# Performance work log

Hardware: AMD Instinct MI355X
Metric: run time of the kernel (lower is better)

## Reference

```python
import jax, jax.numpy as jnp
import numpy as np
from math import factorial

# (mul, l, parity) per irrep; parity +1 = even (e), -1 = odd (o)
IRREPS_IN  = [(64, 0, 1), (32, 1, -1), (16, 2, 1)]
IRREPS_OUT = [(64, 0, 1), (32, 1, -1), (16, 2, 1)]
B = 20000


def _su2_cg(j1, m1, j2, m2, j3, m3):
    # Standard SU(2) Clebsch-Gordan coefficient <j1 m1 j2 m2 | j3 m3> (integer j).
    if m3 != m1 + m2:
        return 0.0
    vmin = max(-j1 + j2 + m3, -j1 + m1, 0)
    vmax = min(j2 + j3 + m1, j3 - j1 + j2, j3 + m3)
    if vmax < vmin:
        return 0.0
    f = factorial
    C = ((2 * j3 + 1) * f(j3 + j1 - j2) * f(j3 - j1 + j2) * f(j1 + j2 - j3)
         * f(j3 + m3) * f(j3 - m3)
         / (f(j1 + j2 + j3 + 1) * f(j1 - m1) * f(j1 + m1) * f(j2 - m2) * f(j2 + m2))) ** 0.5
    S = 0.0
    for v in range(vmin, vmax + 1):
        S += ((-1.0) ** (v + j2 + m2) * f(j2 + j3 + m1 - v) * f(j1 - m1 + v)
              / (f(v) * f(j3 - j1 + j2 - v) * f(j3 + m3 - v) * f(v + j1 - j2 - m3)))
    return C * S


def _q(l):
    # Real -> complex spherical-harmonics change of basis, phased so real CG is real (e3nn convention).
    q = np.zeros((2 * l + 1, 2 * l + 1), dtype=np.complex128)
    for m in range(-l, 0):
        q[l + m, l + abs(m)] = 2 ** -0.5
        q[l + m, l - abs(m)] = -1j * 2 ** -0.5
    q[l, l] = 1.0
    for m in range(1, l + 1):
        q[l + m, l + abs(m)] = (-1) ** m * 2 ** -0.5
        q[l + m, l - abs(m)] = 1j * (-1) ** m * 2 ** -0.5
    return (-1j) ** l * q


def _clebsch_gordan(l1, l2, l3):
    # Real-basis CG coefficients, shape (2l1+1, 2l2+1, 2l3+1).
    C = np.zeros((2 * l1 + 1, 2 * l2 + 1, 2 * l3 + 1), dtype=np.complex128)
    for m1 in range(-l1, l1 + 1):
        for m2 in range(-l2, l2 + 1):
            for m3 in range(-l3, l3 + 1):
                C[l1 + m1, l2 + m2, l3 + m3] = _su2_cg(l1, m1, l2, m2, l3, m3)
    Q1, Q2, Q3 = _q(l1), _q(l2), _q(l3)
    Cr = np.einsum('ij,kl,mn,ikn->jlm', Q1, Q2, np.conj(Q3.T), C)
    return np.real(Cr)


def _build():
    # Enumerate all allowed 'uvw' CG paths (i1, i2, i_out); one learned weight per path.
    ins, cgs = [], []
    for i1, (m1, l1, p1) in enumerate(IRREPS_IN):
        for i2, (m2, l2, p2) in enumerate(IRREPS_IN):
            for lo in range(abs(l1 - l2), l1 + l2 + 1):
                po = p1 * p2
                for io, (mo, l3, p3) in enumerate(IRREPS_OUT):
                    if l3 == lo and p3 == po:
                        ins.append((i1, i2, io, (m1, m2, mo)))
                        # 'component' normalization: scale so each output component has unit variance per path
                        cgs.append((_clebsch_gordan(l1, l2, l3) * (2 * l3 + 1) ** 0.5).astype(np.float32))
                        break
    fan = {}
    for (i1, i2, io, (m1, m2, mo)) in ins:
        fan[io] = fan.get(io, 0) + m1 * m2
    alphas = [1.0 / float(np.sqrt(fan[io])) for (_, _, io, _) in ins]
    return ins, cgs, alphas


INSTRUCTIONS, CGS, ALPHAS = _build()  # 11 instructions for these irreps
DIM_IN = sum(m * (2 * l + 1) for m, l, _ in IRREPS_IN)


def setup_inputs() -> dict:
    key = jax.random.key(0)
    keys = jax.random.split(key, 1 + len(INSTRUCTIONS))
    inp = {"x": jax.random.normal(keys[0], (B, DIM_IN), dtype=jnp.float32)}
    for i, (ins, k) in enumerate(zip(INSTRUCTIONS, keys[1:])):
        inp[f"w{i}"] = jax.random.normal(k, ins[3], dtype=jnp.float32)
    return inp


def _tensor_square(x, ws):
    b = x.shape[0]
    xs, off = [], 0
    for m, l, _ in IRREPS_IN:
        d = m * (2 * l + 1)
        xs.append(x[:, off:off + d].reshape(b, m, 2 * l + 1))
        off += d
    outs = [jnp.zeros((b, m, 2 * l + 1), x.dtype) for m, l, _ in IRREPS_OUT]
    for (i1, i2, io, _), w, C, a in zip(INSTRUCTIONS, ws, CGS, ALPHAS):
        # per-path weighted CG contraction: out[b,w,k] = sum_{u,v,i,j} W[u,v,w] C[i,j,k] x[b,u,i] x[b,v,j]
        contrib = jnp.einsum('uvw,ijk,bui,bvj->bwk', w, jnp.asarray(C, x.dtype),
                             xs[i1], xs[i2], optimize='optimal')
        outs[io] = outs[io] + jnp.asarray(a, x.dtype) * contrib
    return jnp.concatenate([o.reshape(b, -1) for o in outs], axis=1)


def reference(x, w0, w1, w2, w3, w4, w5, w6, w7, w8, w9, w10):
    return _tensor_square(x, (w0, w1, w2, w3, w4, w5, w6, w7, w8, w9, w10))
```

## Files before the change

kernel.cpp:

```cpp
#include <hip/hip_runtime.h>
#include <stdint.h>
#include <stddef.h>


namespace cg {

struct Cx { double re, im; };
constexpr Cx cmul(Cx a, Cx b){ return { a.re*b.re - a.im*b.im, a.re*b.im + a.im*b.re }; }

constexpr double fact(int n){ double r = 1.0; for (int i = 2; i <= n; ++i) r *= (double)i; return r; }

constexpr double csqrt(double x){
  if (x <= 0.0) return 0.0;
  double r = x > 1.0 ? x : 1.0;
  for (int i = 0; i < 50; ++i) r = 0.5*(r + x/r);
  return r;
}

constexpr double neg1pow(int k){ return (k % 2 == 0) ? 1.0 : -1.0; }

constexpr double su2_cg(int j1,int m1,int j2,int m2,int j3,int m3){
  if (m3 != m1 + m2) return 0.0;
  int vmin = -j1 + j2 + m3;
  if (-j1 + m1 > vmin) vmin = -j1 + m1;
  if (0 > vmin) vmin = 0;
  int vmax = j2 + j3 + m1;
  if (j3 - j1 + j2 < vmax) vmax = j3 - j1 + j2;
  if (j3 + m3 < vmax) vmax = j3 + m3;
  if (vmax < vmin) return 0.0;
  double C = csqrt((2.0*j3 + 1.0)*fact(j3+j1-j2)*fact(j3-j1+j2)*fact(j1+j2-j3)
                   *fact(j3+m3)*fact(j3-m3)
                   /(fact(j1+j2+j3+1)*fact(j1-m1)*fact(j1+m1)*fact(j2-m2)*fact(j2+m2)));
  double S = 0.0;
  for (int v = vmin; v <= vmax; ++v)
    S += neg1pow(v + j2 + m2)*fact(j2+j3+m1-v)*fact(j1-m1+v)
       /(fact(v)*fact(j3-j1+j2-v)*fact(j3+m3-v)*fact(v+j1-j2-m3));
  return C*S;
}

struct QM { Cx v[5][5]; };
constexpr QM qmat(int l){
  QM q{};
  const double r2 = 0.70710678118654752440;
  for (int m = -l; m < 0; ++m){
    q.v[l+m][l-m] = Cx{ r2, 0.0 };
    q.v[l+m][l+m] = Cx{ 0.0, -r2 };
  }
  q.v[l][l] = Cx{ 1.0, 0.0 };
  for (int m = 1; m <= l; ++m){
    double s = neg1pow(m)*r2;
    q.v[l+m][l+m] = Cx{ s, 0.0 };
    q.v[l+m][l-m] = Cx{ 0.0, s };
  }
  Cx ph = (l % 4 == 0) ? Cx{1,0} : (l % 4 == 1) ? Cx{0,-1} : (l % 4 == 2) ? Cx{-1,0} : Cx{0,1};
  QM out{};
  for (int i = 0; i < 5; ++i) for (int j = 0; j < 5; ++j) out.v[i][j] = cmul(ph, q.v[i][j]);
  return out;
}

struct CGT { double v[5][5][5]; };
constexpr CGT cg_tab(int l1,int l2,int l3){
  double C[5][5][5] = {};
  for (int m1 = -l1; m1 <= l1; ++m1)
    for (int m2 = -l2; m2 <= l2; ++m2)
      for (int m3 = -l3; m3 <= l3; ++m3)
        C[l1+m1][l2+m2][l3+m3] = su2_cg(l1,m1,l2,m2,l3,m3);
  QM Q1 = qmat(l1), Q2 = qmat(l2), Q3 = qmat(l3);
  const int n1 = 2*l1+1, n2 = 2*l2+1, n3 = 2*l3+1;
  const double norm = csqrt(2.0*l3 + 1.0);
  CGT R{};
  for (int j = 0; j < n1; ++j)
    for (int l = 0; l < n2; ++l)
      for (int m = 0; m < n3; ++m){
        Cx s{0,0};
        for (int i = 0; i < n1; ++i)
          for (int k = 0; k < n2; ++k)
            for (int n = 0; n < n3; ++n){
              double c = C[i][k][n];
              if (c != 0.0){
                Cx q3c{ Q3.v[n][m].re, -Q3.v[n][m].im };
                Cx t = cmul(cmul(Q1.v[i][j], Q2.v[k][l]), q3c);
                s.re += t.re*c; s.im += t.im*c;
              }
            }
        R.v[j][l][m] = s.re * norm;
      }
  return R;
}

constexpr double tab_sumsq(const CGT& t, int n1, int n2, int n3){
  double s = 0;
  for (int i = 0; i < n1; ++i) for (int j = 0; j < n2; ++j) for (int k = 0; k < n3; ++k)
    s += t.v[i][j][k]*t.v[i][j][k];
  return s;
}

}

constexpr cg::CGT T121 = cg::cg_tab(1,2,1);
constexpr cg::CGT T211 = cg::cg_tab(2,1,1);
constexpr cg::CGT T112 = cg::cg_tab(1,1,2);
constexpr cg::CGT T222 = cg::cg_tab(2,2,2);
constexpr double C000 = cg::cg_tab(0,0,0).v[0][0][0];
constexpr double C011 = cg::cg_tab(0,1,1).v[0][0][0];
constexpr double C022 = cg::cg_tab(0,2,2).v[0][0][0];
constexpr double C101 = cg::cg_tab(1,0,1).v[0][0][0];
constexpr double C110 = cg::cg_tab(1,1,0).v[0][0][0];
constexpr double C220 = cg::cg_tab(2,2,0).v[0][0][0];
constexpr double C202 = cg::cg_tab(2,0,2).v[0][0][0];

static_assert(C000 > 0.99 && C000 < 1.01, "C000");
static_assert(C011 > 1.72 && C011 < 1.74, "C011");
static_assert(C101 > 1.72 && C101 < 1.74, "C101");
static_assert(C022 > 2.22 && C022 < 2.25, "C022");
static_assert(C202 > 2.22 && C202 < 2.25, "C202");
static_assert(C110*C110 > 0.332 && C110*C110 < 0.334, "C110");
static_assert(C220*C220 > 0.199 && C220*C220 < 0.201, "C220");
static_assert(cg::tab_sumsq(T121,3,5,3) > 8.9  && cg::tab_sumsq(T121,3,5,3) < 9.1,  "T121");
static_assert(cg::tab_sumsq(T211,5,3,3) > 8.9  && cg::tab_sumsq(T211,5,3,3) < 9.1,  "T211");
static_assert(cg::tab_sumsq(T112,3,3,5) > 24.9 && cg::tab_sumsq(T112,3,3,5) < 25.1, "T112");
static_assert(cg::tab_sumsq(T222,5,5,5) > 24.9 && cg::tab_sumsq(T222,5,5,5) < 25.1, "T222");

constexpr double t121_t211_swapdiff(){
  double m = 0;
  for (int i = 0; i < 5; ++i)
    for (int j = 0; j < 3; ++j)
      for (int k = 0; k < 3; ++k){
        double d = T211.v[i][j][k] - T121.v[j][i][k];
        if (d < 0) d = -d;
        if (d > m) m = d;
      }
  return m;
}
static_assert(t121_t211_swapdiff() < 1e-9, "T211 != T121^T -- fold invalid");

constexpr double A0 = 1.0/cg::csqrt(5376.0);
constexpr double A1 = 1.0/cg::csqrt(5120.0);
constexpr double A2 = 1.0/cg::csqrt(3328.0);

constexpr double S000 = A0*C000, S110 = A0*C110, S220 = A0*C220;
constexpr double S011 = A1*C011, S101 = A1*C101, S121 = A1, S211 = A1;
constexpr double S022 = A2*C022, S112 = A2,      S202 = A2*C202, S222 = A2;

constexpr int K0 = 4352, K1 = 2560, K2 = 2304;
constexpr int WT1_OFF = 64*K0;
constexpr int WT2_OFF = WT1_OFF + 32*K1;

using short8  = __attribute__((ext_vector_type(8))) short;
using float4v = __attribute__((ext_vector_type(4))) float;

__device__ __forceinline__ unsigned pkbf(float lo, float hi){
  unsigned a = __builtin_bit_cast(unsigned, lo);
  unsigned b = __builtin_bit_cast(unsigned, hi);
  return __builtin_amdgcn_perm(b, a, 0x07060302u);
}

__device__ __forceinline__ short8 mkfrag(const float* s){
  union { short8 v; unsigned u[4]; } f;
  f.u[0] = pkbf(s[0], s[1]);
  f.u[1] = pkbf(s[2], s[3]);
  f.u[2] = pkbf(s[4], s[5]);
  f.u[3] = pkbf(s[6], s[7]);
  return f.v;
}

__device__ __forceinline__ short8 ldB(const unsigned short* p){
  return *reinterpret_cast<const short8*>(p);
}

__device__ __forceinline__ float4v MFMA(short8 a, short8 b, float4v c){
  return __builtin_amdgcn_mfma_f32_16x16x32_bf16(a, b, c, 0, 0, 0);
}

__device__ __forceinline__ unsigned short f2bf_rne(float f){
  unsigned u = __builtin_bit_cast(unsigned, f);
  u += 0x7fffu + ((u >> 16) & 1u);
  return (unsigned short)(u >> 16);
}

#define NZ(c) ((c) > 1e-12 || (c) < -1e-12)

constexpr int XS = 244;

__global__ __launch_bounds__(256)
void tsq_prep(const float* __restrict__ w0, const float* __restrict__ w1,
              const float* __restrict__ w2, const float* __restrict__ w3,
              const float* __restrict__ w4, const float* __restrict__ w5,
              const float* __restrict__ w6, const float* __restrict__ w7,
              const float* __restrict__ w8, const float* __restrict__ w9,
              const float* __restrict__ w10, unsigned short* __restrict__ wt){
  const int s   = blockIdx.x;
  const int g   = blockIdx.y;
  const int tid = threadIdx.x;

  const int lw  = 6 - g;
  const int Wn  = 1 << lw;
  const int NT  = Wn >> 4;
  int Smax;
  unsigned short* obase;
  if (g == 0){ Smax = 136; obase = wt; }
  else if (g == 1){ Smax = 80; obase = wt + WT1_OFF; }
  else { Smax = 72; obase = wt + WT2_OFF; }
  if (s >= Smax) return;

  __shared__ unsigned short tl[32*66];
  const int st = Wn + 2;

  const int nel = 32 << lw;
  for (int idx = tid; idx < nel; idx += 256){
    const int kk = idx >> lw, n = idx & (Wn - 1);
    float v;
    if (g == 0){
      if (s < 64){
        const int u = s >> 1, vv = (s & 1)*32 + kk;
        v = w0[(u*64 + vv)*64 + n];
        if (s & 1) v += w0[(vv*64 + u)*64 + n];
        v *= (float)S000;
      } else if (s < 96){
        const int u = s - 32, vv = 32 + kk;
        v = w0[(u*64 + vv)*64 + n] * (float)S000;
      } else if (s < 128){
        v = w4[((s-96)*32 + kk)*64 + n] * (float)S110;
      } else {
        v = w9[((s-128)*32 + kk)*64 + n] * (float)S220;
      }
    } else if (g == 1){
      const int k = s*32 + kk;
      if (s < 64){
        v = w1[((k&63)*32 + (k>>6))*32 + n] * (float)S011
          + w3[k*32 + n] * (float)S101;
      } else {
        const int kr = k - 2048;
        const int u1 = kr & 31, v2 = kr >> 5;
        v = w6[(u1*16 + v2)*32 + n] * (float)S121
          + w8[(v2*32 + u1)*32 + n] * (float)S211;
      }
    } else {
      const int k = s*32 + kk;
      if (s < 32){
        v = w2[((k&63)*16 + (k>>6))*16 + n] * (float)S022
          + w7[k*16 + n] * (float)S202;
      } else if (s < 64){
        v = w5[(k-1024)*16 + n] * (float)S112;
      } else {
        v = w10[(k-2048)*16 + n] * (float)S222;
      }
    }
    tl[kk*st + n] = f2bf_rne(v);
  }
  __syncthreads();

  unsigned short* o = obase + (size_t)s*NT*512;
  const int nout = NT*512;
  for (int idx = tid; idx < nout; idx += 256){
    const int nt  = idx >> 9;
    const int r   = idx & 511;
    const int col = r >> 5;
    const int kk  = r & 31;
    o[idx] = tl[kk*st + nt*16 + col];
  }
}

__global__ __launch_bounds__(512, 4)
void tsq_main(const float* __restrict__ x, const unsigned short* __restrict__ wt,
              float* __restrict__ out){
  __shared__ float lx[64*XS];
  const int g    = blockIdx.x;
  const int b0   = blockIdx.y * 64;
  const int tid  = threadIdx.x;
  const int wv   = tid >> 6;
  const int lane = tid & 63;
  const int col  = lane & 15;
  const int tg   = lane >> 4;
  const int fo   = col*32 + tg*8;

  for (int i = tid; i < 64*60; i += 512){
    const int r = i / 60, c = i - r*60;
    int gb = b0 + r; if (gb > 19999) gb = 19999;
    const float4 v = *(reinterpret_cast<const float4*>(x + (size_t)gb*240) + c);
    *reinterpret_cast<float4*>(&lx[r*XS + c*4]) = v;
  }
  __syncthreads();

  const float4v z4 = {0.f, 0.f, 0.f, 0.f};

  if (g == 0){
    const unsigned short* bpl = wt + fo;
    const int mh  = wv >> 2;
    const int kh  = wv & 3;
    const int par = kh & 1;

    float4v acc[2][4];
    #pragma unroll
    for (int mt = 0; mt < 2; ++mt)
      #pragma unroll
      for (int nt = 0; nt < 4; ++nt) acc[mt][nt] = z4;

    const float* rbase[2];
    #pragma unroll
    for (int mt = 0; mt < 2; ++mt) rbase[mt] = &lx[(mh*32 + mt*16 + col)*XS];

    float wA[2][8], wB[2][8];
    #pragma unroll
    for (int mt = 0; mt < 2; ++mt){
      const float4 a0 = *reinterpret_cast<const float4*>(rbase[mt] + par*32 + tg*8);
      const float4 a1 = *reinterpret_cast<const float4*>(rbase[mt] + par*32 + tg*8 + 4);
      wA[mt][0]=a0.x; wA[mt][1]=a0.y; wA[mt][2]=a0.z; wA[mt][3]=a0.w;
      wA[mt][4]=a1.x; wA[mt][5]=a1.y; wA[mt][6]=a1.z; wA[mt][7]=a1.w;
      const float4 b0v = *reinterpret_cast<const float4*>(rbase[mt] + 32 + tg*8);
      const float4 b1v = *reinterpret_cast<const float4*>(rbase[mt] + 32 + tg*8 + 4);
      wB[mt][0]=b0v.x; wB[mt][1]=b0v.y; wB[mt][2]=b0v.z; wB[mt][3]=b0v.w;
      wB[mt][4]=b1v.x; wB[mt][5]=b1v.y; wB[mt][6]=b1v.z; wB[mt][7]=b1v.w;
    }

    for (int s = kh; s < 64; s += 4){
      short8 bf[4];
      #pragma unroll
      for (int nt = 0; nt < 4; ++nt) bf[nt] = ldB(bpl + (s*4 + nt)*512);
      const int u = s >> 1;
      #pragma unroll
      for (int mt = 0; mt < 2; ++mt){
        const float xu = rbase[mt][u];
        float sv[8];
        #pragma unroll
        for (int t = 0; t < 8; ++t) sv[t] = xu * wA[mt][t];
        const short8 af = mkfrag(sv);
        #pragma unroll
        for (int nt = 0; nt < 4; ++nt) acc[mt][nt] = MFMA(af, bf[nt], acc[mt][nt]);
      }
    }
    for (int s = 64 + kh; s < 96; s += 4){
      short8 bf[4];
      #pragma unroll
      for (int nt = 0; nt < 4; ++nt) bf[nt] = ldB(bpl + (s*4 + nt)*512);
      const int u = s - 32;
      #pragma unroll
      for (int mt = 0; mt < 2; ++mt){
        const float xu = rbase[mt][u];
        float sv[8];
        #pragma unroll
        for (int t = 0; t < 8; ++t) sv[t] = xu * wB[mt][t];
        const short8 af = mkfrag(sv);
        #pragma unroll
        for (int nt = 0; nt < 4; ++nt) acc[mt][nt] = MFMA(af, bf[nt], acc[mt][nt]);
      }
    }
    float x1w[2][24];
    #pragma unroll
    for (int mt = 0; mt < 2; ++mt)
      #pragma unroll
      for (int q = 0; q < 6; ++q){
        const float4 v = *reinterpret_cast<const float4*>(rbase[mt] + 64 + tg*24 + q*4);
        x1w[mt][q*4+0] = v.x; x1w[mt][q*4+1] = v.y;
        x1w[mt][q*4+2] = v.z; x1w[mt][q*4+3] = v.w;
      }
    for (int s = 96 + kh; s < 128; s += 4){
      short8 bf[4];
      #pragma unroll
      for (int nt = 0; nt < 4; ++nt) bf[nt] = ldB(bpl + (s*4 + nt)*512);
      const int u = s - 96;
      #pragma unroll
      for (int mt = 0; mt < 2; ++mt){
        const float* rb = rbase[mt];
        const float u0 = rb[64+u*3], u1 = rb[64+u*3+1], u2 = rb[64+u*3+2];
        float sv[8];
        #pragma unroll
        for (int t = 0; t < 8; ++t)
          sv[t] = fmaf(u0, x1w[mt][t*3], fmaf(u1, x1w[mt][t*3+1], u2*x1w[mt][t*3+2]));
        const short8 af = mkfrag(sv);
        #pragma unroll
        for (int nt = 0; nt < 4; ++nt) acc[mt][nt] = MFMA(af, bf[nt], acc[mt][nt]);
      }
    }
    for (int s = 128 + kh; s < 136; s += 4){
      short8 bf[4];
      #pragma unroll
      for (int nt = 0; nt < 4; ++nt) bf[nt] = ldB(bpl + (s*4 + nt)*512);
      const int ub = (s - 128)*2 + (tg >> 1);
      #pragma unroll
      for (int mt = 0; mt < 2; ++mt){
        const float* rb = rbase[mt];
        float xu[5];
        #pragma unroll
        for (int i = 0; i < 5; ++i) xu[i] = rb[160 + ub*5 + i];
        float xv[40];
        #pragma unroll
        for (int q = 0; q < 10; ++q){
          const float4 v = *reinterpret_cast<const float4*>(rb + 160 + (tg&1)*40 + q*4);
          xv[q*4+0] = v.x; xv[q*4+1] = v.y; xv[q*4+2] = v.z; xv[q*4+3] = v.w;
        }
        float sv[8];
        #pragma unroll
        for (int t = 0; t < 8; ++t){
          float a = 0.f;
          #pragma unroll
          for (int i = 0; i < 5; ++i) a = fmaf(xu[i], xv[t*5+i], a);
          sv[t] = a;
        }
        const short8 af = mkfrag(sv);
        #pragma unroll
        for (int nt = 0; nt < 4; ++nt) acc[mt][nt] = MFMA(af, bf[nt], acc[mt][nt]);
      }
    }
    __syncthreads();
    float* red = lx;
    if (kh != 0){
      #pragma unroll
      for (int mt = 0; mt < 2; ++mt)
        #pragma unroll
        for (int nt = 0; nt < 4; ++nt)
          #pragma unroll
          for (int r = 0; r < 4; ++r)
            red[mh*6144 + ((kh-1)*8 + mt*4 + nt)*256 + (tg*4 + r)*16 + col] = acc[mt][nt][r];
    }
    __syncthreads();
    if (kh == 0){
      #pragma unroll
      for (int mt = 0; mt < 2; ++mt)
        #pragma unroll
        for (int r = 0; r < 4; ++r){
          const int b = b0 + mh*32 + mt*16 + tg*4 + r;
          if (b < 20000){
            #pragma unroll
            for (int nt = 0; nt < 4; ++nt){
              float v = acc[mt][nt][r];
              #pragma unroll
              for (int w2 = 1; w2 < 4; ++w2)
                v += red[mh*6144 + ((w2-1)*8 + mt*4 + nt)*256 + (tg*4 + r)*16 + col];
              out[(size_t)b*240 + nt*16 + col] = v;
            }
          }
        }
    }

  } else if (g == 1){
    const unsigned short* bpl = wt + WT1_OFF + fo;
    const int mq = wv >> 1;
    const int kh = wv & 1;
    const float* rb = &lx[(mq*16 + col)*XS];

    float4v acc[3][2];
    #pragma unroll
    for (int k3 = 0; k3 < 3; ++k3)
      #pragma unroll
      for (int nt = 0; nt < 2; ++nt) acc[k3][nt] = z4;

    float w8[8];
    {
      const float4 v0 = *reinterpret_cast<const float4*>(rb + kh*32 + tg*8);
      const float4 v1 = *reinterpret_cast<const float4*>(rb + kh*32 + tg*8 + 4);
      w8[0]=v0.x; w8[1]=v0.y; w8[2]=v0.z; w8[3]=v0.w;
      w8[4]=v1.x; w8[5]=v1.y; w8[6]=v1.z; w8[7]=v1.w;
    }
    float x1w[24];
    #pragma unroll
    for (int q = 0; q < 6; ++q){
      const float4 v = *reinterpret_cast<const float4*>(rb + 64 + tg*24 + q*4);
      x1w[q*4+0] = v.x; x1w[q*4+1] = v.y; x1w[q*4+2] = v.z; x1w[q*4+3] = v.w;
    }

    for (int s = kh; s < 64; s += 2){
      const short8 bf0 = ldB(bpl + (s*2    )*512);
      const short8 bf1 = ldB(bpl + (s*2 + 1)*512);
      const int m = s >> 1;
      const float c0 = rb[64+m*3], c1 = rb[64+m*3+1], c2 = rb[64+m*3+2];
      float sv0[8], sv1[8], sv2[8];
      #pragma unroll
      for (int t = 0; t < 8; ++t){
        const float xw = w8[t];
        sv0[t] = xw*c0; sv1[t] = xw*c1; sv2[t] = xw*c2;
      }
      const short8 a0 = mkfrag(sv0), a1 = mkfrag(sv1), a2 = mkfrag(sv2);
      acc[0][0] = MFMA(a0, bf0, acc[0][0]);
      acc[0][1] = MFMA(a0, bf1, acc[0][1]);
      acc[1][0] = MFMA(a1, bf0, acc[1][0]);
      acc[1][1] = MFMA(a1, bf1, acc[1][1]);
      acc[2][0] = MFMA(a2, bf0, acc[2][0]);
      acc[2][1] = MFMA(a2, bf1, acc[2][1]);
    }
    for (int s = 64 + kh; s < 80; s += 2){
      const short8 bf0 = ldB(bpl + (s*2    )*512);
      const short8 bf1 = ldB(bpl + (s*2 + 1)*512);
      const int v2 = s - 64;
      float xq[5];
      #pragma unroll
      for (int j = 0; j < 5; ++j) xq[j] = rb[160 + v2*5 + j];
      float t3[3][3];
      #pragma unroll
      for (int kk = 0; kk < 3; ++kk)
        #pragma unroll
        for (int i = 0; i < 3; ++i){
          float a = 0.f;
          #pragma unroll
          for (int j = 0; j < 5; ++j){
            const double cd = T121.v[i][j][kk];
            if (NZ(cd)) a = fmaf((float)cd, xq[j], a);
          }
          t3[kk][i] = a;
        }
      float sv0[8], sv1[8], sv2[8];
      #pragma unroll
      for (int t = 0; t < 8; ++t){
        const float a0_ = x1w[t*3], a1_ = x1w[t*3+1], a2_ = x1w[t*3+2];
        sv0[t] = fmaf(a0_, t3[0][0], fmaf(a1_, t3[0][1], a2_*t3[0][2]));
        sv1[t] = fmaf(a0_, t3[1][0], fmaf(a1_, t3[1][1], a2_*t3[1][2]));
        sv2[t] = fmaf(a0_, t3[2][0], fmaf(a1_, t3[2][1], a2_*t3[2][2]));
      }
      const short8 a0 = mkfrag(sv0), a1 = mkfrag(sv1), a2 = mkfrag(sv2);
      acc[0][0] = MFMA(a0, bf0, acc[0][0]);
      acc[0][1] = MFMA(a0, bf1, acc[0][1]);
      acc[1][0] = MFMA(a1, bf0, acc[1][0]);
      acc[1][1] = MFMA(a1, bf1, acc[1][1]);
      acc[2][0] = MFMA(a2, bf0, acc[2][0]);
      acc[2][1] = MFMA(a2, bf1, acc[2][1]);
    }
    __syncthreads();
    float* red = lx;
    if (kh == 1){
      #pragma unroll
      for (int k3 = 0; k3 < 3; ++k3)
        #pragma unroll
        for (int nt = 0; nt < 2; ++nt)
          #pragma unroll
          for (int r = 0; r < 4; ++r)
            red[mq*1536 + (k3*2 + nt)*256 + (tg*4 + r)*16 + col] = acc[k3][nt][r];
    }
    __syncthreads();
    if (kh == 0){
      #pragma unroll
      for (int r = 0; r < 4; ++r){
        const int b = b0 + mq*16 + tg*4 + r;
        if (b < 20000){
          #pragma unroll
          for (int nt = 0; nt < 2; ++nt){
            const int w2 = nt*16 + col;
            float* o = out + (size_t)b*240 + 64 + 3*w2;
            #pragma unroll
            for (int k3 = 0; k3 < 3; ++k3)
              o[k3] = acc[k3][nt][r]
                    + red[mq*1536 + (k3*2 + nt)*256 + (tg*4 + r)*16 + col];
          }
        }
      }
    }

  } else {
    const unsigned short* bpl = wt + WT2_OFF + fo;
    const int mq = wv >> 1;
    const int kh = wv & 1;
    const float* rb = &lx[(mq*16 + col)*XS];

    float4v acc[5] = { z4, z4, z4, z4, z4 };

    float w8[8];
    {
      const float4 v0 = *reinterpret_cast<const float4*>(rb + kh*32 + tg*8);
      const float4 v1 = *reinterpret_cast<const float4*>(rb + kh*32 + tg*8 + 4);
      w8[0]=v0.x; w8[1]=v0.y; w8[2]=v0.z; w8[3]=v0.w;
      w8[4]=v1.x; w8[5]=v1.y; w8[6]=v1.z; w8[7]=v1.w;
    }
    float x1w[24];
    #pragma unroll
    for (int q = 0; q < 6; ++q){
      const float4 v = *reinterpret_cast<const float4*>(rb + 64 + tg*24 + q*4);
      x1w[q*4+0] = v.x; x1w[q*4+1] = v.y; x1w[q*4+2] = v.z; x1w[q*4+3] = v.w;
    }

    for (int s = kh; s < 32; s += 2){
      const short8 bf = ldB(bpl + s*512);
      const int v2 = s >> 1;
      float xq[5];
      #pragma unroll
      for (int j = 0; j < 5; ++j) xq[j] = rb[160 + v2*5 + j];
      float sv[5][8];
      #pragma unroll
      for (int t = 0; t < 8; ++t){
        const float xw = w8[t];
        #pragma unroll
        for (int k5 = 0; k5 < 5; ++k5) sv[k5][t] = xw * xq[k5];
      }
      #pragma unroll
      for (int k5 = 0; k5 < 5; ++k5) acc[k5] = MFMA(mkfrag(sv[k5]), bf, acc[k5]);
    }
    for (int s = 32 + kh; s < 64; s += 2){
      const short8 bf = ldB(bpl + s*512);
      const int u = s - 32;
      float xu[3];
      #pragma unroll
      for (int i = 0; i < 3; ++i) xu[i] = rb[64 + u*3 + i];
      float t5[5][3];
      #pragma unroll
      for (int kk = 0; kk < 5; ++kk)
        #pragma unroll
        for (int j = 0; j < 3; ++j){
          float a = 0.f;
          #pragma unroll
          for (int i = 0; i < 3; ++i){
            const double cd = T112.v[i][j][kk];
            if (NZ(cd)) a = fmaf((float)cd, xu[i], a);
          }
          t5[kk][j] = a;
        }
      float sv[5][8];
      #pragma unroll
      for (int t = 0; t < 8; ++t){
        const float b0_ = x1w[t*3], b1_ = x1w[t*3+1], b2_ = x1w[t*3+2];
        #pragma unroll
        for (int kk = 0; kk < 5; ++kk)
          sv[kk][t] = fmaf(b0_, t5[kk][0], fmaf(b1_, t5[kk][1], b2_*t5[kk][2]));
      }
      #pragma unroll
      for (int k5 = 0; k5 < 5; ++k5) acc[k5] = MFMA(mkfrag(sv[k5]), bf, acc[k5]);
    }
    float x2w[40];
    #pragma unroll
    for (int q = 0; q < 10; ++q){
      const float4 v = *reinterpret_cast<const float4*>(rb + 160 + (tg&1)*40 + q*4);
      x2w[q*4+0] = v.x; x2w[q*4+1] = v.y; x2w[q*4+2] = v.z; x2w[q*4+3] = v.w;
    }
    for (int s = 64 + kh; s < 72; s += 2){
      const short8 bf = ldB(bpl + s*512);
      const int ub = (s - 64)*2 + (tg >> 1);
      float xu[5];
      #pragma unroll
      for (int i = 0; i < 5; ++i) xu[i] = rb[160 + ub*5 + i];
      float t5[5][5];
      #pragma unroll
      for (int kk = 0; kk < 5; ++kk)
        #pragma unroll
        for (int j = 0; j < 5; ++j){
          float a = 0.f;
          #pragma unroll
          for (int i = 0; i < 5; ++i){
            const double cd = T222.v[i][j][kk];
            if (NZ(cd)) a = fmaf((float)cd, xu[i], a);
          }
          t5[kk][j] = a;
        }
      float sv[5][8];
      #pragma unroll
      for (int t = 0; t < 8; ++t){
        #pragma unroll
        for (int kk = 0; kk < 5; ++kk){
          float a = 0.f;
          #pragma unroll
          for (int j = 0; j < 5; ++j) a = fmaf(x2w[t*5+j], t5[kk][j], a);
          sv[kk][t] = a;
        }
      }
      #pragma unroll
      for (int k5 = 0; k5 < 5; ++k5) acc[k5] = MFMA(mkfrag(sv[k5]), bf, acc[k5]);
    }
    __syncthreads();
    float* red = lx;
    if (kh == 1){
      #pragma unroll
      for (int k5 = 0; k5 < 5; ++k5)
        #pragma unroll
        for (int r = 0; r < 4; ++r)
          red[mq*1280 + k5*256 + (tg*4 + r)*16 + col] = acc[k5][r];
    }
    __syncthreads();
    if (kh == 0){
      #pragma unroll
      for (int r = 0; r < 4; ++r){
        const int b = b0 + mq*16 + tg*4 + r;
        if (b < 20000){
          float* o = out + (size_t)b*240 + 160 + 5*col;
          #pragma unroll
          for (int k5 = 0; k5 < 5; ++k5)
            o[k5] = acc[k5][r] + red[mq*1280 + k5*256 + (tg*4 + r)*16 + col];
        }
      }
    }
  }
}

extern "C" void kernel_launch(void* const* d_in, const int* in_sizes, int n_in,
                              void* d_out, int out_size, void* d_ws, size_t ws_size,
                              hipStream_t stream){
  (void)in_sizes; (void)n_in; (void)out_size; (void)ws_size;
  const float* x = (const float*)d_in[0];
  const float* w[11];
  for (int i = 0; i < 11; ++i) w[i] = (const float*)d_in[1 + i];
  unsigned short* wt = (unsigned short*)d_ws;
  float* out = (float*)d_out;

  dim3 gp(136, 3);
  tsq_prep<<<gp, 256, 0, stream>>>(w[0], w[1], w[2], w[3], w[4], w[5],
                                   w[6], w[7], w[8], w[9], w[10], wt);
  dim3 gm(3, 313);
  tsq_main<<<gm, 512, 0, stream>>>(x, wt, out);
}
```

Measured before the change: 167.8 us.

## Stage x in LDS as bf16, serialize reduction, raise occupancy to six blocks

```diff
diff --git a/kernel.cpp b/kernel.cpp
--- a/kernel.cpp
+++ b/kernel.cpp
@@ -150,9 +150,9 @@
 using float4v = __attribute__((ext_vector_type(4))) float;
 
 __device__ __forceinline__ unsigned pkbf(float lo, float hi){
-  unsigned a = __builtin_bit_cast(unsigned, lo);
-  unsigned b = __builtin_bit_cast(unsigned, hi);
-  return __builtin_amdgcn_perm(b, a, 0x07060302u);
+  unsigned r;
+  asm("v_cvt_pk_bf16_f32 %0, %1, %2" : "=v"(r) : "v"(lo), "v"(hi));
+  return r;
 }
 
 __device__ __forceinline__ short8 mkfrag(const float* s){
@@ -178,9 +178,24 @@
   return (unsigned short)(u >> 16);
 }
 
+__device__ __forceinline__ float bf2f(unsigned short h){
+  return __builtin_bit_cast(float, (unsigned)h << 16);
+}
+
+template<int N>
+__device__ __forceinline__ void ldw(const unsigned short* p, float* dst){
+  #pragma unroll
+  for (int q = 0; q < N/8; ++q){
+    union { short8 v; unsigned short u[8]; } t;
+    t.v = *reinterpret_cast<const short8*>(p + q*8);
+    #pragma unroll
+    for (int i = 0; i < 8; ++i) dst[q*8 + i] = bf2f(t.u[i]);
+  }
+}
+
 #define NZ(c) ((c) > 1e-12 || (c) < -1e-12)
 
-constexpr int XS = 244;
+constexpr int XSH = 248;
 
 __global__ __launch_bounds__(256)
 void tsq_prep(const float* __restrict__ w0, const float* __restrict__ w1,
@@ -261,10 +276,10 @@
   }
 }
 
-__global__ __launch_bounds__(512, 4)
+__global__ __launch_bounds__(512, 6)
 void tsq_main(const float* __restrict__ x, const unsigned short* __restrict__ wt,
               float* __restrict__ out){
-  __shared__ float lx[64*XS];
+  __shared__ unsigned short lxh[64*XSH];
   const int g    = blockIdx.x;
   const int b0   = blockIdx.y * 64;
   const int tid  = threadIdx.x;
@@ -278,7 +293,8 @@
     const int r = i / 60, c = i - r*60;
     int gb = b0 + r; if (gb > 19999) gb = 19999;
     const float4 v = *(reinterpret_cast<const float4*>(x + (size_t)gb*240) + c);
-    *reinterpret_cast<float4*>(&lx[r*XS + c*4]) = v;
+    uint2 p; p.x = pkbf(v.x, v.y); p.y = pkbf(v.z, v.w);
+    *reinterpret_cast<uint2*>(&lxh[r*XSH + c*4]) = p;
   }
   __syncthreads();
 
@@ -296,21 +312,15 @@
       #pragma unroll
       for (int nt = 0; nt < 4; ++nt) acc[mt][nt] = z4;
 
-    const float* rbase[2];
+    const unsigned short* rbase[2];
     #pragma unroll
-    for (int mt = 0; mt < 2; ++mt) rbase[mt] = &lx[(mh*32 + mt*16 + col)*XS];
+    for (int mt = 0; mt < 2; ++mt) rbase[mt] = &lxh[(mh*32 + mt*16 + col)*XSH];
 
     float wA[2][8], wB[2][8];
     #pragma unroll
     for (int mt = 0; mt < 2; ++mt){
-      const float4 a0 = *reinterpret_cast<const float4*>(rbase[mt] + par*32 + tg*8);
-      const float4 a1 = *reinterpret_cast<const float4*>(rbase[mt] + par*32 + tg*8 + 4);
-      wA[mt][0]=a0.x; wA[mt][1]=a0.y; wA[mt][2]=a0.z; wA[mt][3]=a0.w;
-      wA[mt][4]=a1.x; wA[mt][5]=a1.y; wA[mt][6]=a1.z; wA[mt][7]=a1.w;
-      const float4 b0v = *reinterpret_cast<const float4*>(rbase[mt] + 32 + tg*8);
-      const float4 b1v = *reinterpret_cast<const float4*>(rbase[mt] + 32 + tg*8 + 4);
-      wB[mt][0]=b0v.x; wB[mt][1]=b0v.y; wB[mt][2]=b0v.z; wB[mt][3]=b0v.w;
-      wB[mt][4]=b1v.x; wB[mt][5]=b1v.y; wB[mt][6]=b1v.z; wB[mt][7]=b1v.w;
+      ldw<8>(rbase[mt] + par*32 + tg*8, wA[mt]);
+      ldw<8>(rbase[mt] + 32 + tg*8,     wB[mt]);
     }
 
     for (int s = kh; s < 64; s += 4){
@@ -320,7 +330,7 @@
       const int u = s >> 1;
       #pragma unroll
       for (int mt = 0; mt < 2; ++mt){
-        const float xu = rbase[mt][u];
+        const float xu = bf2f(rbase[mt][u]);
         float sv[8];
         #pragma unroll
         for (int t = 0; t < 8; ++t) sv[t] = xu * wA[mt][t];
@@ -336,7 +346,7 @@
       const int u = s - 32;
       #pragma unroll
       for (int mt = 0; mt < 2; ++mt){
-        const float xu = rbase[mt][u];
+        const float xu = bf2f(rbase[mt][u]);
         float sv[8];
         #pragma unroll
         for (int t = 0; t < 8; ++t) sv[t] = xu * wB[mt][t];
@@ -347,13 +357,7 @@
     }
     float x1w[2][24];
     #pragma unroll
-    for (int mt = 0; mt < 2; ++mt)
-      #pragma unroll
-      for (int q = 0; q < 6; ++q){
-        const float4 v = *reinterpret_cast<const float4*>(rbase[mt] + 64 + tg*24 + q*4);
-        x1w[mt][q*4+0] = v.x; x1w[mt][q*4+1] = v.y;
-        x1w[mt][q*4+2] = v.z; x1w[mt][q*4+3] = v.w;
-      }
+    for (int mt = 0; mt < 2; ++mt) ldw<24>(rbase[mt] + 64 + tg*24, x1w[mt]);
     for (int s = 96 + kh; s < 128; s += 4){
       short8 bf[4];
       #pragma unroll
@@ -361,8 +365,8 @@
       const int u = s - 96;
       #pragma unroll
       for (int mt = 0; mt < 2; ++mt){
-        const float* rb = rbase[mt];
-        const float u0 = rb[64+u*3], u1 = rb[64+u*3+1], u2 = rb[64+u*3+2];
+        const unsigned short* rb = rbase[mt];
+        const float u0 = bf2f(rb[64+u*3]), u1 = bf2f(rb[64+u*3+1]), u2 = bf2f(rb[64+u*3+2]);
         float sv[8];
         #pragma unroll
         for (int t = 0; t < 8; ++t)
@@ -372,48 +376,60 @@
         for (int nt = 0; nt < 4; ++nt) acc[mt][nt] = MFMA(af, bf[nt], acc[mt][nt]);
       }
     }
-    for (int s = 128 + kh; s < 136; s += 4){
-      short8 bf[4];
-      #pragma unroll
-      for (int nt = 0; nt < 4; ++nt) bf[nt] = ldB(bpl + (s*4 + nt)*512);
-      const int ub = (s - 128)*2 + (tg >> 1);
-      #pragma unroll
-      for (int mt = 0; mt < 2; ++mt){
-        const float* rb = rbase[mt];
-        float xu[5];
-        #pragma unroll
-        for (int i = 0; i < 5; ++i) xu[i] = rb[160 + ub*5 + i];
-        float xv[40];
-        #pragma unroll
-        for (int q = 0; q < 10; ++q){
-          const float4 v = *reinterpret_cast<const float4*>(rb + 160 + (tg&1)*40 + q*4);
-          xv[q*4+0] = v.x; xv[q*4+1] = v.y; xv[q*4+2] = v.z; xv[q*4+3] = v.w;
+    {
+      float xv[2][40];
+      #pragma unroll
+      for (int mt = 0; mt < 2; ++mt) ldw<40>(rbase[mt] + 160 + (tg&1)*40, xv[mt]);
+      for (int s = 128 + kh; s < 136; s += 4){
+        short8 bf[4];
+        #pragma unroll
+        for (int nt = 0; nt < 4; ++nt) bf[nt] = ldB(bpl + (s*4 + nt)*512);
+        const int ub = (s - 128)*2 + (tg >> 1);
+        #pragma unroll
+        for (int mt = 0; mt < 2; ++mt){
+          const unsigned short* rb = rbase[mt];
+          float xu[5];
+          #pragma unroll
+          for (int i = 0; i < 5; ++i) xu[i] = bf2f(rb[160 + ub*5 + i]);
+          float sv[8];
+          #pragma unroll
+          for (int t = 0; t < 8; ++t){
+            float a = 0.f;
+            #pragma unroll
+            for (int i = 0; i < 5; ++i) a = fmaf(xu[i], xv[mt][t*5+i], a);
+            sv[t] = a;
+          }
+          const short8 af = mkfrag(sv);
+          #pragma unroll
+          for (int nt = 0; nt < 4; ++nt) acc[mt][nt] = MFMA(af, bf[nt], acc[mt][nt]);
         }
-        float sv[8];
-        #pragma unroll
-        for (int t = 0; t < 8; ++t){
-          float a = 0.f;
-          #pragma unroll
-          for (int i = 0; i < 5; ++i) a = fmaf(xu[i], xv[t*5+i], a);
-          sv[t] = a;
-        }
-        const short8 af = mkfrag(sv);
-        #pragma unroll
-        for (int nt = 0; nt < 4; ++nt) acc[mt][nt] = MFMA(af, bf[nt], acc[mt][nt]);
       }
     }
     __syncthreads();
-    float* red = lx;
-    if (kh != 0){
-      #pragma unroll
-      for (int mt = 0; mt < 2; ++mt)
-        #pragma unroll
-        for (int nt = 0; nt < 4; ++nt)
-          #pragma unroll
-          for (int r = 0; r < 4; ++r)
-            red[mh*6144 + ((kh-1)*8 + mt*4 + nt)*256 + (tg*4 + r)*16 + col] = acc[mt][nt][r];
-    }
-    __syncthreads();
+    float* red = reinterpret_cast<float*>(lxh);
+    #pragma unroll
+    for (int p = 1; p <= 3; ++p){
+      if (kh == p){
+        #pragma unroll
+        for (int mt = 0; mt < 2; ++mt)
+          #pragma unroll
+          for (int nt = 0; nt < 4; ++nt)
+            #pragma unroll
+            for (int r = 0; r < 4; ++r)
+              red[mh*2048 + (mt*4 + nt)*256 + (tg*4 + r)*16 + col] = acc[mt][nt][r];
+      }
+      __syncthreads();
+      if (kh == 0){
+        #pragma unroll
+        for (int mt = 0; mt < 2; ++mt)
+          #pragma unroll
+          for (int nt = 0; nt < 4; ++nt)
+            #pragma unroll
+            for (int r = 0; r < 4; ++r)
+              acc[mt][nt][r] += red[mh*2048 + (mt*4 + nt)*256 + (tg*4 + r)*16 + col];
+      }
+      __syncthreads();
+    }
     if (kh == 0){
       #pragma unroll
       for (int mt = 0; mt < 2; ++mt)
@@ -422,13 +438,8 @@
           const int b = b0 + mh*32 + mt*16 + tg*4 + r;
           if (b < 20000){
             #pragma unroll
-            for (int nt = 0; nt < 4; ++nt){
-              float v = acc[mt][nt][r];
-              #pragma unroll
-              for (int w2 = 1; w2 < 4; ++w2)
-                v += red[mh*6144 + ((w2-1)*8 + mt*4 + nt)*256 + (tg*4 + r)*16 + col];
-              out[(size_t)b*240 + nt*16 + col] = v;
-            }
+            for (int nt = 0; nt < 4; ++nt)
+              out[(size_t)b*240 + nt*16 + col] = acc[mt][nt][r];
           }
         }
     }
@@ -437,7 +448,7 @@
     const unsigned short* bpl = wt + WT1_OFF + fo;
     const int mq = wv >> 1;
     const int kh = wv & 1;
-    const float* rb = &lx[(mq*16 + col)*XS];
+    const unsigned short* rb = &lxh[(mq*16 + col)*XSH];
 
     float4v acc[3][2];
     #pragma unroll
@@ -446,24 +457,15 @@
       for (int nt = 0; nt < 2; ++nt) acc[k3][nt] = z4;
 
     float w8[8];
-    {
-      const float4 v0 = *reinterpret_cast<const float4*>(rb + kh*32 + tg*8);
-      const float4 v1 = *reinterpret_cast<const float4*>(rb + kh*32 + tg*8 + 4);
-      w8[0]=v0.x; w8[1]=v0.y; w8[2]=v0.z; w8[3]=v0.w;
-      w8[4]=v1.x; w8[5]=v1.y; w8[6]=v1.z; w8[7]=v1.w;
-    }
+    ldw<8>(rb + kh*32 + tg*8, w8);
     float x1w[24];
-    #pragma unroll
-    for (int q = 0; q < 6; ++q){
-      const float4 v = *reinterpret_cast<const float4*>(rb + 64 + tg*24 + q*4);
-      x1w[q*4+0] = v.x; x1w[q*4+1] = v.y; x1w[q*4+2] = v.z; x1w[q*4+3] = v.w;
-    }
+    ldw<24>(rb + 64 + tg*24, x1w);
 
     for (int s = kh; s < 64; s += 2){
       const short8 bf0 = ldB(bpl + (s*2    )*512);
       const short8 bf1 = ldB(bpl + (s*2 + 1)*512);
       const int m = s >> 1;
-      const float c0 = rb[64+m*3], c1 = rb[64+m*3+1], c2 = rb[64+m*3+2];
+      const float c0 = bf2f(rb[64+m*3]), c1 = bf2f(rb[64+m*3+1]), c2 = bf2f(rb[64+m*3+2]);
       float sv0[8], sv1[8], sv2[8];
       #pragma unroll
       for (int t = 0; t < 8; ++t){
@@ -484,7 +486,7 @@
       const int v2 = s - 64;
       float xq[5];
       #pragma unroll
-      for (int j = 0; j < 5; ++j) xq[j] = rb[160 + v2*5 + j];
+      for (int j = 0; j < 5; ++j) xq[j] = bf2f(rb[160 + v2*5 + j]);
       float t3[3][3];
       #pragma unroll
       for (int kk = 0; kk < 3; ++kk)
@@ -515,7 +517,7 @@
       acc[2][1] = MFMA(a2, bf1, acc[2][1]);
     }
     __syncthreads();
-    float* red = lx;
+    float* red = reinterpret_cast<float*>(lxh);
     if (kh == 1){
       #pragma unroll
       for (int k3 = 0; k3 < 3; ++k3)
@@ -548,30 +550,21 @@
     const unsigned short* bpl = wt + WT2_OFF + fo;
     const int mq = wv >> 1;
     const int kh = wv & 1;
-    const float* rb = &lx[(mq*16 + col)*XS];
+    const unsigned short* rb = &lxh[(mq*16 + col)*XSH];
 
     float4v acc[5] = { z4, z4, z4, z4, z4 };
 
     float w8[8];
-    {
-      const float4 v0 = *reinterpret_cast<const float4*>(rb + kh*32 + tg*8);
-      const float4 v1 = *reinterpret_cast<const float4*>(rb + kh*32 + tg*8 + 4);
-      w8[0]=v0.x; w8[1]=v0.y; w8[2]=v0.z; w8[3]=v0.w;
-      w8[4]=v1.x; w8[5]=v1.y; w8[6]=v1.z; w8[7]=v1.w;
-    }
+    ldw<8>(rb + kh*32 + tg*8, w8);
     float x1w[24];
-    #pragma unroll
-    for (int q = 0; q < 6; ++q){
-      const float4 v = *reinterpret_cast<const float4*>(rb + 64 + tg*24 + q*4);
-      x1w[q*4+0] = v.x; x1w[q*4+1] = v.y; x1w[q*4+2] = v.z; x1w[q*4+3] = v.w;
-    }
+    ldw<24>(rb + 64 + tg*24, x1w);
 
     for (int s = kh; s < 32; s += 2){
       const short8 bf = ldB(bpl + s*512);
       const int v2 = s >> 1;
       float xq[5];
       #pragma unroll
-      for (int j = 0; j < 5; ++j) xq[j] = rb[160 + v2*5 + j];
+      for (int j = 0; j < 5; ++j) xq[j] = bf2f(rb[160 + v2*5 + j]);
       float sv[5][8];
       #pragma unroll
       for (int t = 0; t < 8; ++t){
@@ -587,7 +580,7 @@
       const int u = s - 32;
       float xu[3];
       #pragma unroll
-      for (int i = 0; i < 3; ++i) xu[i] = rb[64 + u*3 + i];
+      for (int i = 0; i < 3; ++i) xu[i] = bf2f(rb[64 + u*3 + i]);
       float t5[5][3];
       #pragma unroll
       for (int kk = 0; kk < 5; ++kk)
@@ -612,47 +605,45 @@
       #pragma unroll
       for (int k5 = 0; k5 < 5; ++k5) acc[k5] = MFMA(mkfrag(sv[k5]), bf, acc[k5]);
     }
-    float x2w[40];
-    #pragma unroll
-    for (int q = 0; q < 10; ++q){
-      const float4 v = *reinterpret_cast<const float4*>(rb + 160 + (tg&1)*40 + q*4);
-      x2w[q*4+0] = v.x; x2w[q*4+1] = v.y; x2w[q*4+2] = v.z; x2w[q*4+3] = v.w;
-    }
-    for (int s = 64 + kh; s < 72; s += 2){
-      const short8 bf = ldB(bpl + s*512);
-      const int ub = (s - 64)*2 + (tg >> 1);
-      float xu[5];
-      #pragma unroll
-      for (int i = 0; i < 5; ++i) xu[i] = rb[160 + ub*5 + i];
-      float t5[5][5];
-      #pragma unroll
-      for (int kk = 0; kk < 5; ++kk)
-        #pragma unroll
-        for (int j = 0; j < 5; ++j){
-          float a = 0.f;
-          #pragma unroll
-          for (int i = 0; i < 5; ++i){
-            const double cd = T222.v[i][j][kk];
-            if (NZ(cd)) a = fmaf((float)cd, xu[i], a);
+    {
+      float x2w[40];
+      ldw<40>(rb + 160 + (tg&1)*40, x2w);
+      for (int s = 64 + kh; s < 72; s += 2){
+        const short8 bf = ldB(bpl + s*512);
+        const int ub = (s - 64)*2 + (tg >> 1);
+        float xu[5];
+        #pragma unroll
+        for (int i = 0; i < 5; ++i) xu[i] = bf2f(rb[160 + ub*5 + i]);
+        float t5[5][5];
+        #pragma unroll
+        for (int kk = 0; kk < 5; ++kk)
+          #pragma unroll
+          for (int j = 0; j < 5; ++j){
+            float a = 0.f;
+            #pragma unroll
+            for (int i = 0; i < 5; ++i){
+              const double cd = T222.v[i][j][kk];
+              if (NZ(cd)) a = fmaf((float)cd, xu[i], a);
+            }
+            t5[kk][j] = a;
           }
-          t5[kk][j] = a;
+        float sv[5][8];
+        #pragma unroll
+        for (int t = 0; t < 8; ++t){
+          #pragma unroll
+          for (int kk = 0; kk < 5; ++kk){
+            float a = 0.f;
+            #pragma unroll
+            for (int j = 0; j < 5; ++j) a = fmaf(x2w[t*5+j], t5[kk][j], a);
+            sv[kk][t] = a;
+          }
         }
-      float sv[5][8];
-      #pragma unroll
-      for (int t = 0; t < 8; ++t){
-        #pragma unroll
-        for (int kk = 0; kk < 5; ++kk){
-          float a = 0.f;
-          #pragma unroll
-          for (int j = 0; j < 5; ++j) a = fmaf(x2w[t*5+j], t5[kk][j], a);
-          sv[kk][t] = a;
-        }
-      }
-      #pragma unroll
-      for (int k5 = 0; k5 < 5; ++k5) acc[k5] = MFMA(mkfrag(sv[k5]), bf, acc[k5]);
+        #pragma unroll
+        for (int k5 = 0; k5 < 5; ++k5) acc[k5] = MFMA(mkfrag(sv[k5]), bf, acc[k5]);
+      }
     }
     __syncthreads();
-    float* red = lx;
+    float* red = reinterpret_cast<float*>(lxh);
     if (kh == 1){
       #pragma unroll
       for (int k5 = 0; k5 < 5; ++k5)
```

Result: slower. 250.7 us (+49.4%).
